# Kernel optimization log

Hardware: AMD Instinct MI355X
Metric: run time of the kernel (lower is better)

## Reference

```python
import jax, jax.numpy as jnp
import numpy as np

N_NODES = 50000
N_EDGES = 1000000
IN_SIZE = 64
OUT_SIZE = 64
EDGE_DIM = 16
BN_EPS = 1e-5
GIN_EPS = 0.0  # GINEConv default eps, train_eps=False


def setup_inputs() -> dict:
    key = jax.random.key(0)
    ks = jax.random.split(key, 10)
    s = 1.0 / np.sqrt(IN_SIZE)
    return {
        "x": jax.random.normal(ks[0], (N_NODES, IN_SIZE), dtype=jnp.float32),
        "edge_index": jax.random.randint(ks[1], (2, N_EDGES), 0, N_NODES, dtype=jnp.int64),
        "edge_attr": jax.random.normal(ks[2], (N_EDGES, EDGE_DIM), dtype=jnp.float32),
        # GINEConv internal edge projection Linear(edge_dim -> in_size)
        "W_edge": jax.random.uniform(ks[3], (IN_SIZE, EDGE_DIM), jnp.float32, -s, s),
        "b_edge": jnp.zeros((IN_SIZE,), jnp.float32),
        # MLP: Linear(in, out) -> BatchNorm1d(out) -> ReLU -> Linear(out, out)
        "W1": jax.random.uniform(ks[4], (OUT_SIZE, IN_SIZE), jnp.float32, -s, s),
        "b1": jnp.zeros((OUT_SIZE,), jnp.float32),
        "gamma": jnp.ones((OUT_SIZE,), jnp.float32),
        "beta": jnp.zeros((OUT_SIZE,), jnp.float32),
        "W2": jax.random.uniform(ks[5], (OUT_SIZE, OUT_SIZE), jnp.float32, -1.0 / np.sqrt(OUT_SIZE), 1.0 / np.sqrt(OUT_SIZE)),
        "b2": jnp.zeros((OUT_SIZE,), jnp.float32),
    }


def reference(x, edge_index, edge_attr, W_edge, b_edge, W1, b1, gamma, beta, W2, b2):
    src = edge_index[0]  # x_j (message source)
    dst = edge_index[1]  # aggregation target
    # project edge attrs to node-feature dim (GINEConv's self.lin)
    ea = edge_attr @ W_edge.T + b_edge                      # [E, d]
    msg = jax.nn.relu(x[src] + ea)                          # [E, d]
    agg = jax.ops.segment_sum(msg, dst, num_segments=x.shape[0])  # [N, d]
    h = (1.0 + GIN_EPS) * x + agg                           # GINE combine
    # MLP with BatchNorm1d (training mode: batch stats, biased var)
    h = h @ W1.T + b1
    mean = jnp.mean(h, axis=0)
    var = jnp.var(h, axis=0)
    h = gamma * (h - mean) * jax.lax.rsqrt(var + BN_EPS) + beta
    h = jax.nn.relu(h)
    return h @ W2.T + b2
```

## Files before the change

### kernel.cpp

```cpp
#include <hip/hip_runtime.h>
#include <hip/hip_fp16.h>

#define NN 50000
#define NE 1000000
#define D  64
#define ED 16
#define CAP 64
#define BN_EPS 1e-5f
#define QSCALE 1048576.0f

#define BSH  8
#define NBKT 196
#define BCAP 6144
#define EPB  4096

struct alignas(16) SE8  { int   v[8];  };
struct alignas(16) F16v { float f[16]; };

__global__ __launch_bounds__(256) void xhalf_kernel(
    const float* __restrict__ x, __half* __restrict__ xh)
{
    const int i = blockIdx.x * 256 + threadIdx.x;
    if (i >= NN * D / 4) return;
    const float4 a = reinterpret_cast<const float4*>(x)[i];
    ushort4 h;
    h.x = __half_as_ushort(__float2half(a.x));
    h.y = __half_as_ushort(__float2half(a.y));
    h.z = __half_as_ushort(__float2half(a.z));
    h.w = __half_as_ushort(__float2half(a.w));
    reinterpret_cast<ushort4*>(xh)[i] = h;
}

__global__ __launch_bounds__(256) void partA_kernel(
    const int*  __restrict__ ei32,
    int*        __restrict__ gcur,
    uint2*      __restrict__ bucketed)
{
    __shared__ uint2 s_staged[EPB];
    __shared__ int s_cnt[NBKT], s_pref[NBKT], s_cnt2[NBKT], s_gbase[NBKT];

    const int tid = threadIdx.x;
    const long long base = (long long)blockIdx.x * EPB;
    const int nedge = (int)((NE - base < EPB) ? (NE - base) : EPB);

    const int hi = ei32[2 * (tid & 63) + 1];
    const bool is64 = !__any(hi != 0);

    for (int i = tid; i < NBKT; i += 256) { s_cnt[i] = 0; s_cnt2[i] = 0; }
    __syncthreads();

    int srcv[16], dstv[16];
    #pragma unroll
    for (int i = 0; i < 16; ++i) {
        const int k = i * 256 + tid;
        int s = 0, d = 0;
        if (k < nedge) {
            const long long e = base + k;
            s = is64 ? ei32[2 * e]        : ei32[e];
            d = is64 ? ei32[2 * (NE + e)] : ei32[NE + e];
            atomicAdd(&s_cnt[d >> BSH], 1);
        }
        srcv[i] = s; dstv[i] = d;
    }
    __syncthreads();

    if (tid < NBKT) s_pref[tid] = s_cnt[tid];
    __syncthreads();
    for (int off = 1; off < NBKT; off <<= 1) {
        int v = 0;
        if (tid < NBKT && tid >= off) v = s_pref[tid - off];
        __syncthreads();
        if (tid < NBKT) s_pref[tid] += v;
        __syncthreads();
    }
    if (tid < NBKT) s_gbase[tid] = atomicAdd(&gcur[tid], s_cnt[tid]);
    __syncthreads();

    #pragma unroll
    for (int i = 0; i < 16; ++i) {
        const int k = i * 256 + tid;
        if (k < nedge) {
            const int d = dstv[i], b = d >> BSH;
            const int r = atomicAdd(&s_cnt2[b], 1);
            const int p = (s_pref[b] - s_cnt[b]) + r;
            s_staged[p] = make_uint2((unsigned)srcv[i] | ((unsigned)d << 16),
                                     (unsigned)(base + k));
        }
    }
    __syncthreads();

    for (int p = tid; p < nedge; p += 256) {
        const uint2 rec = s_staged[p];
        const int d = (int)(rec.x >> 16), b = d >> BSH;
        const int local = p - (s_pref[b] - s_cnt[b]);
        const int gpos = s_gbase[b] + local;
        if (gpos < BCAP)
            bucketed[(size_t)b * BCAP + gpos] = rec;
    }
}

__global__ __launch_bounds__(512) void partB_kernel(
    const uint2* __restrict__ bucketed,
    const int*   __restrict__ gcur,
    int*         __restrict__ cursor,
    int2*        __restrict__ padded)
{
    __shared__ int s_deg[1 << BSH];
    const int tid = threadIdx.x;
    const int b = blockIdx.x;

    for (int i = tid; i < (1 << BSH); i += 512) s_deg[i] = 0;
    __syncthreads();

    const int cnt = min(gcur[b], BCAP);
    const uint2* reg = bucketed + (size_t)b * BCAP;
    for (int k = tid; k < cnt; k += 512) {
        const uint2 rec = reg[k];
        const int src = (int)(rec.x & 0xffffu);
        const int dst = (int)(rec.x >> 16);
        const int slot = atomicAdd(&s_deg[dst & ((1 << BSH) - 1)], 1);
        if (slot < CAP)
            padded[(size_t)dst * CAP + slot] = make_int2(src, (int)rec.y);
    }
    __syncthreads();
    for (int i = tid; i < (1 << BSH); i += 512) {
        const int n = (b << BSH) + i;
        if (n < NN) cursor[n] = s_deg[i];
    }
}

__global__ __launch_bounds__(256) void scatter_kernel(
    const int* __restrict__ ei32,
    int*       __restrict__ cursor,
    int2*      __restrict__ padded)
{
    const int e = blockIdx.x * 256 + threadIdx.x;
    const int hi = ei32[2 * (threadIdx.x & 63) + 1];
    const bool is64 = !__any(hi != 0);
    if (e >= NE) return;
    const int src = is64 ? ei32[2 * e]        : ei32[e];
    const int dst = is64 ? ei32[2 * (NE + e)] : ei32[NE + e];
    const int slot = atomicAdd(&cursor[dst], 1);
    if (slot < CAP) padded[(size_t)dst * CAP + slot] = make_int2(src, e);
}

template<bool XH>
__global__ __launch_bounds__(256) void gather_kernel(
    const int2*  __restrict__ padded,
    const int*   __restrict__ cursor,
    const float* __restrict__ x,
    const __half* __restrict__ xh,
    const float* __restrict__ ea,
    const float* __restrict__ W_edge,
    const float* __restrict__ b_edge,
    float*       __restrict__ agg,
    int n0, int n1)
{
    const int tid  = threadIdx.x;
    const int lane = tid & 63;
    const int n = __builtin_amdgcn_readfirstlane(n0 + blockIdx.x * 4 + (tid >> 6));
    if (n >= n1) return;

    float wv[ED];
    #pragma unroll
    for (int i = 0; i < ED / 4; ++i) {
        float4 t = reinterpret_cast<const float4*>(W_edge)[lane * (ED / 4) + i];
        wv[4*i+0] = t.x; wv[4*i+1] = t.y; wv[4*i+2] = t.z; wv[4*i+3] = t.w;
    }
    const float bo = b_edge[lane];

    const int deg = __builtin_amdgcn_readfirstlane(min(cursor[n], CAP));
    const int2* row = padded + (size_t)n * CAP;

    int iacc = 0;
    for (int e0 = 0; e0 < deg; e0 += 4) {
        const SE8 g = *reinterpret_cast<const SE8*>(row + e0);

        const bool l1 = (e0 + 1 < deg), l2 = (e0 + 2 < deg), l3 = (e0 + 3 < deg);
        const int src0 = __builtin_amdgcn_readfirstlane(g.v[0]);
        const int eid0 = __builtin_amdgcn_readfirstlane(g.v[1]);
        const int src1 = __builtin_amdgcn_readfirstlane(l1 ? g.v[2] : g.v[0]);
        const int eid1 = __builtin_amdgcn_readfirstlane(l1 ? g.v[3] : g.v[1]);
        const int src2 = __builtin_amdgcn_readfirstlane(l2 ? g.v[4] : g.v[0]);
        const int eid2 = __builtin_amdgcn_readfirstlane(l2 ? g.v[5] : g.v[1]);
        const int src3 = __builtin_amdgcn_readfirstlane(l3 ? g.v[6] : g.v[0]);
        const int eid3 = __builtin_amdgcn_readfirstlane(l3 ? g.v[7] : g.v[1]);

        const F16v a0 = *reinterpret_cast<const F16v*>(ea + (size_t)eid0 * ED);
        const F16v a1 = *reinterpret_cast<const F16v*>(ea + (size_t)eid1 * ED);
        const F16v a2 = *reinterpret_cast<const F16v*>(ea + (size_t)eid2 * ED);
        const F16v a3 = *reinterpret_cast<const F16v*>(ea + (size_t)eid3 * ED);

        float xv0, xv1, xv2, xv3;
        if (XH) {
            xv0 = __half2float(xh[(size_t)src0 * D + lane]);
            xv1 = __half2float(xh[(size_t)src1 * D + lane]);
            xv2 = __half2float(xh[(size_t)src2 * D + lane]);
            xv3 = __half2float(xh[(size_t)src3 * D + lane]);
        } else {
            xv0 = x[(size_t)src0 * D + lane];
            xv1 = x[(size_t)src1 * D + lane];
            xv2 = x[(size_t)src2 * D + lane];
            xv3 = x[(size_t)src3 * D + lane];
        }

        float d0 = bo, d1 = bo, d2 = bo, d3 = bo;
        #pragma unroll
        for (int k = 0; k < ED; ++k) {
            d0 += a0.f[k] * wv[k];
            d1 += a1.f[k] * wv[k];
            d2 += a2.f[k] * wv[k];
            d3 += a3.f[k] * wv[k];
        }
        iacc += __float2int_rn(fmaxf(d0 + xv0, 0.f) * QSCALE);
        iacc += l1 ? __float2int_rn(fmaxf(d1 + xv1, 0.f) * QSCALE) : 0;
        iacc += l2 ? __float2int_rn(fmaxf(d2 + xv2, 0.f) * QSCALE) : 0;
        iacc += l3 ? __float2int_rn(fmaxf(d3 + xv3, 0.f) * QSCALE) : 0;
    }
    agg[(size_t)n * D + lane] = (float)iacc * (1.0f / QSCALE);
}

__global__ __launch_bounds__(256) void edge_kernel(
    const float* __restrict__ x,
    const int*   __restrict__ ei32,
    const float* __restrict__ ea,
    const float* __restrict__ W_edge,
    const float* __restrict__ b_edge,
    float*       __restrict__ agg)
{
    __shared__ float s_ea[64 * ED];
    __shared__ int   s_src[64];
    __shared__ int   s_dst[64];

    const int tid  = threadIdx.x;
    const int lane = tid & 63;
    const int wave = tid >> 6;
    const long long ebase = (long long)blockIdx.x * 64;

    const int hi = ei32[2 * lane + 1];
    const bool is64 = !__any(hi != 0);

    float w[ED];
    #pragma unroll
    for (int i = 0; i < ED / 4; ++i) {
        float4 t = reinterpret_cast<const float4*>(W_edge)[lane * (ED / 4) + i];
        w[4*i+0] = t.x; w[4*i+1] = t.y; w[4*i+2] = t.z; w[4*i+3] = t.w;
    }
    const float bo = b_edge[lane];

    reinterpret_cast<float4*>(s_ea)[tid] =
        reinterpret_cast<const float4*>(ea + ebase * ED)[tid];

    if (tid < 64) {
        long long e = ebase + tid;
        s_src[tid] = is64 ? ei32[2 * e] : ei32[e];
    } else if (tid < 128) {
        long long e = ebase + (tid - 64);
        s_dst[tid - 64] = is64 ? ei32[2 * (NE + e)] : ei32[NE + e];
    }
    __syncthreads();

    #pragma unroll 4
    for (int i = 0; i < 16; ++i) {
        const int el = wave * 16 + i;
        float acc = bo;
        const float* er = s_ea + el * ED;
        #pragma unroll
        for (int k = 0; k < ED; ++k) acc += er[k] * w[k];
        const long long s = s_src[el];
        const long long d = s_dst[el];
        float m = fmaxf(acc + x[s * D + lane], 0.f);
        atomicAdd(&agg[d * D + lane], m);
    }
}


__global__ __launch_bounds__(256) void node1_kernel(
    const float* __restrict__ x,
    const float* __restrict__ agg,
    const float* __restrict__ W1,
    const float* __restrict__ b1,
    float*       __restrict__ h1,
    float*       __restrict__ colsum,
    float*       __restrict__ colsumsq)
{
    __shared__ float s_h[64 * D];
    const int tid  = threadIdx.x;
    const int o    = tid & 63;
    const int wave = tid >> 6;
    const long long rbase = (long long)blockIdx.x * 64;

    float w[D];
    #pragma unroll
    for (int i = 0; i < D / 4; ++i) {
        float4 t = reinterpret_cast<const float4*>(W1)[o * (D / 4) + i];
        w[4*i+0] = t.x; w[4*i+1] = t.y; w[4*i+2] = t.z; w[4*i+3] = t.w;
    }

    #pragma unroll
    for (int i = 0; i < 4; ++i) {
        const int f4 = tid + 256 * i;
        const long long row = rbase + (f4 >> 4);
        float4 t = make_float4(0.f, 0.f, 0.f, 0.f);
        if (row < NN) {
            float4 a = reinterpret_cast<const float4*>(x)  [row * (D/4) + (f4 & 15)];
            float4 g = reinterpret_cast<const float4*>(agg)[row * (D/4) + (f4 & 15)];
            t.x = a.x + g.x; t.y = a.y + g.y; t.z = a.z + g.z; t.w = a.w + g.w;
        }
        reinterpret_cast<float4*>(s_h)[f4] = t;
    }
    __syncthreads();

    const float bb = b1[o];
    float psum = 0.f, psq = 0.f;
    for (int i = 0; i < 16; ++i) {
        const int r = wave + 4 * i;
        const long long row = rbase + r;
        float acc = bb;
        const float4* sr = reinterpret_cast<const float4*>(s_h + r * D);
        #pragma unroll
        for (int k = 0; k < D / 4; ++k) {
            float4 v = sr[k];
            acc += v.x * w[4*k+0] + v.y * w[4*k+1] + v.z * w[4*k+2] + v.w * w[4*k+3];
        }
        if (row < NN) {
            h1[row * D + o] = acc;
            psum += acc;
            psq  += acc * acc;
        }
    }
    __syncthreads();
    s_h[wave * 64 + o]       = psum;
    s_h[256 + wave * 64 + o] = psq;
    __syncthreads();
    if (tid < 64) {
        float s0 = s_h[tid] + s_h[64 + tid] + s_h[128 + tid] + s_h[192 + tid];
        float q0 = s_h[256 + tid] + s_h[320 + tid] + s_h[384 + tid] + s_h[448 + tid];
        atomicAdd(&colsum[tid], s0);
        atomicAdd(&colsumsq[tid], q0);
    }
}

__global__ void bnstats_kernel(
    const float* __restrict__ colsum,
    const float* __restrict__ colsumsq,
    const float* __restrict__ gamma,
    const float* __restrict__ beta,
    float*       __restrict__ scale,
    float*       __restrict__ shift)
{
    const int o = threadIdx.x;
    const float inv_n = 1.f / (float)NN;
    const float mean = colsum[o] * inv_n;
    const float var  = colsumsq[o] * inv_n - mean * mean;
    const float sc   = gamma[o] * rsqrtf(var + BN_EPS);
    scale[o] = sc;
    shift[o] = beta[o] - mean * sc;
}

__global__ __launch_bounds__(256) void node2_kernel(
    const float* __restrict__ h1,
    const float* __restrict__ scale,
    const float* __restrict__ shift,
    const float* __restrict__ W2,
    const float* __restrict__ b2,
    float*       __restrict__ out)
{
    __shared__ float s_a[64 * D];
    __shared__ float s_sc[D];
    __shared__ float s_sh[D];
    const int tid  = threadIdx.x;
    const int o    = tid & 63;
    const int wave = tid >> 6;
    const long long rbase = (long long)blockIdx.x * 64;

    if (tid < D) { s_sc[tid] = scale[tid]; s_sh[tid] = shift[tid]; }

    float w[D];
    #pragma unroll
    for (int i = 0; i < D / 4; ++i) {
        float4 t = reinterpret_cast<const float4*>(W2)[o * (D / 4) + i];
        w[4*i+0] = t.x; w[4*i+1] = t.y; w[4*i+2] = t.z; w[4*i+3] = t.w;
    }
    __syncthreads();

    #pragma unroll
    for (int i = 0; i < 4; ++i) {
        const int f4 = tid + 256 * i;
        const long long row = rbase + (f4 >> 4);
        float4 t = make_float4(0.f, 0.f, 0.f, 0.f);
        if (row < NN) {
            float4 v = reinterpret_cast<const float4*>(h1)[row * (D/4) + (f4 & 15)];
            const int c = (f4 & 15) * 4;
            t.x = fmaxf(v.x * s_sc[c+0] + s_sh[c+0], 0.f);
            t.y = fmaxf(v.y * s_sc[c+1] + s_sh[c+1], 0.f);
            t.z = fmaxf(v.z * s_sc[c+2] + s_sh[c+2], 0.f);
            t.w = fmaxf(v.w * s_sc[c+3] + s_sh[c+3], 0.f);
        }
        reinterpret_cast<float4*>(s_a)[f4] = t;
    }
    __syncthreads();

    const float bb = b2[o];
    for (int i = 0; i < 16; ++i) {
        const int r = wave + 4 * i;
        const long long row = rbase + r;
        float acc = bb;
        const float4* sr = reinterpret_cast<const float4*>(s_a + r * D);
        #pragma unroll
        for (int k = 0; k < D / 4; ++k) {
            float4 v = sr[k];
            acc += v.x * w[4*k+0] + v.y * w[4*k+1] + v.z * w[4*k+2] + v.w * w[4*k+3];
        }
        if (row < NN) out[row * D + o] = acc;
    }
}


extern "C" void kernel_launch(void* const* d_in, const int* in_sizes, int n_in,
                              void* d_out, int out_size, void* d_ws, size_t ws_size,
                              hipStream_t stream)
{
    const float* x      = (const float*)d_in[0];
    const int*   ei32   = (const int*)  d_in[1];
    const float* ea     = (const float*)d_in[2];
    const float* W_edge = (const float*)d_in[3];
    const float* b_edge = (const float*)d_in[4];
    const float* W1     = (const float*)d_in[5];
    const float* b1     = (const float*)d_in[6];
    const float* gamma  = (const float*)d_in[7];
    const float* beta   = (const float*)d_in[8];
    const float* W2     = (const float*)d_in[9];
    const float* b2     = (const float*)d_in[10];
    float* out = (float*)d_out;

    float*  agg      = (float*)d_ws;
    float*  h1       = agg + (size_t)NN * D;
    int*    cursor   = (int*)(h1 + (size_t)NN * D);
    float*  colsum   = (float*)(cursor + NN);
    float*  colsumsq = colsum + 64;
    float*  scale    = colsumsq + 64;
    float*  shift    = scale + 64;
    int2*   padded   = (int2*)(shift + 64);
    __half* xh       = (__half*)(padded + (size_t)NN * CAP);
    int*    gcur     = (int*)(xh + (size_t)NN * D);
    uint2*  bucketed = (uint2*)h1;

    const size_t need_base = (size_t)(2 * NN * D + NN + 256) * 4 + (size_t)NN * CAP * 8;
    const size_t need_xh   = need_base + (size_t)NN * D * 2;
    const size_t need_rx   = need_xh + (size_t)NBKT * 4;

    if (ws_size >= need_rx) {
        hipMemsetAsync(gcur, 0, (size_t)NBKT * 4, stream);
        hipMemsetAsync(colsum, 0, 256 * 4, stream);
        xhalf_kernel<<<(NN * D / 4 + 255) / 256, 256, 0, stream>>>(x, xh);
        partA_kernel<<<(NE + EPB - 1) / EPB, 256, 0, stream>>>(ei32, gcur, bucketed);
        partB_kernel<<<NBKT, 512, 0, stream>>>(bucketed, gcur, cursor, padded);
        gather_kernel<true><<<NN / 8, 256, 0, stream>>>(padded, cursor, x, xh, ea, W_edge, b_edge, agg, 0, NN / 2);
        gather_kernel<true><<<NN / 8, 256, 0, stream>>>(padded, cursor, x, xh, ea, W_edge, b_edge, agg, NN / 2, NN);
    } else if (ws_size >= need_base) {
        hipMemsetAsync(cursor, 0, (size_t)(NN + 256) * 4, stream);
        scatter_kernel<<<(NE + 255) / 256, 256, 0, stream>>>(ei32, cursor, padded);
        gather_kernel<false><<<NN / 8, 256, 0, stream>>>(padded, cursor, x, xh, ea, W_edge, b_edge, agg, 0, NN / 2);
        gather_kernel<false><<<NN / 8, 256, 0, stream>>>(padded, cursor, x, xh, ea, W_edge, b_edge, agg, NN / 2, NN);
    } else {
        hipMemsetAsync(agg, 0, (size_t)NN * D * 4, stream);
        hipMemsetAsync(cursor, 0, (size_t)(NN + 256) * 4, stream);
        edge_kernel<<<NE / 64, 256, 0, stream>>>(x, ei32, ea, W_edge, b_edge, agg);
    }
    node1_kernel<<<(NN + 63) / 64, 256, 0, stream>>>(x, agg, W1, b1, h1, colsum, colsumsq);
    bnstats_kernel<<<1, 64, 0, stream>>>(colsum, colsumsq, gamma, beta, scale, shift);
    node2_kernel<<<(NN + 63) / 64, 256, 0, stream>>>(h1, scale, shift, W2, b2, out);
}
```

Measured before the change: 172.3 us.

## Pack edge attrs to fp16, use fdot2 gather with software pipelining, finer buckets

Adds a pack kernel that converts both x and edge_attr to fp16 in one pass. A new gather kernel reads the fp16 edge attributes and computes the edge projection with packed fp16 dot products, double-buffering the loads of the next edge group. It also halves the bucket width and edges-per-block in the radix partition, launches partA with 512 threads, and merges the two half-range gather launches into one. The intent is to cut the gather's memory traffic and instruction count, at the cost of an extra full pass over edge_attr, more workspace, and reduced precision in the edge projection.

```diff
diff --git a/kernel.cpp b/kernel.cpp
--- a/kernel.cpp
+++ b/kernel.cpp
@@ -9,13 +9,44 @@
 #define BN_EPS 1e-5f
 #define QSCALE 1048576.0f
 
-#define BSH  8
-#define NBKT 196
-#define BCAP 6144
-#define EPB  4096
-
-struct alignas(16) SE8  { int   v[8];  };
+#define BSH  7
+#define NBKT 391
+#define BCAP 3072
+#define EPB  2048
+
+typedef _Float16 f16;
+typedef _Float16 f16x2 __attribute__((ext_vector_type(2)));
+
+struct alignas(16) SE8  { int v[8]; };
+struct alignas(16) H16  { unsigned u[8]; };
 struct alignas(16) F16v { float f[16]; };
+
+__global__ __launch_bounds__(256) void pack_kernel(
+    const float* __restrict__ x, const float* __restrict__ ea,
+    __half* __restrict__ xh, __half* __restrict__ eah)
+{
+    const long long NX  = (long long)NN * D / 4;
+    const long long NEA = (long long)NE * ED / 4;
+    const long long i = (long long)blockIdx.x * 256 + threadIdx.x;
+    if (i < NX) {
+        const float4 a = reinterpret_cast<const float4*>(x)[i];
+        ushort4 h;
+        h.x = __half_as_ushort(__float2half(a.x));
+        h.y = __half_as_ushort(__float2half(a.y));
+        h.z = __half_as_ushort(__float2half(a.z));
+        h.w = __half_as_ushort(__float2half(a.w));
+        reinterpret_cast<ushort4*>(xh)[i] = h;
+    } else if (i < NX + NEA) {
+        const long long j = i - NX;
+        const float4 a = reinterpret_cast<const float4*>(ea)[j];
+        ushort4 h;
+        h.x = __half_as_ushort(__float2half(a.x));
+        h.y = __half_as_ushort(__float2half(a.y));
+        h.z = __half_as_ushort(__float2half(a.z));
+        h.w = __half_as_ushort(__float2half(a.w));
+        reinterpret_cast<ushort4*>(eah)[j] = h;
+    }
+}
 
 __global__ __launch_bounds__(256) void xhalf_kernel(
     const float* __restrict__ x, __half* __restrict__ xh)
@@ -31,7 +62,7 @@
     reinterpret_cast<ushort4*>(xh)[i] = h;
 }
 
-__global__ __launch_bounds__(256) void partA_kernel(
+__global__ __launch_bounds__(512) void partA_kernel(
     const int*  __restrict__ ei32,
     int*        __restrict__ gcur,
     uint2*      __restrict__ bucketed)
@@ -41,18 +72,18 @@
 
     const int tid = threadIdx.x;
     const long long base = (long long)blockIdx.x * EPB;
-    const int nedge = (int)((NE - base < EPB) ? (NE - base) : EPB);
+    const int nedge = (int)(((long long)NE - base < EPB) ? (NE - base) : EPB);
 
     const int hi = ei32[2 * (tid & 63) + 1];
     const bool is64 = !__any(hi != 0);
 
-    for (int i = tid; i < NBKT; i += 256) { s_cnt[i] = 0; s_cnt2[i] = 0; }
-    __syncthreads();
-
-    int srcv[16], dstv[16];
-    #pragma unroll
-    for (int i = 0; i < 16; ++i) {
-        const int k = i * 256 + tid;
+    for (int i = tid; i < NBKT; i += 512) { s_cnt[i] = 0; s_cnt2[i] = 0; }
+    __syncthreads();
+
+    int srcv[4], dstv[4];
+    #pragma unroll
+    for (int i = 0; i < 4; ++i) {
+        const int k = i * 512 + tid;
         int s = 0, d = 0;
         if (k < nedge) {
             const long long e = base + k;
@@ -77,8 +108,8 @@
     __syncthreads();
 
     #pragma unroll
-    for (int i = 0; i < 16; ++i) {
-        const int k = i * 256 + tid;
+    for (int i = 0; i < 4; ++i) {
+        const int k = i * 512 + tid;
         if (k < nedge) {
             const int d = dstv[i], b = d >> BSH;
             const int r = atomicAdd(&s_cnt2[b], 1);
@@ -89,7 +120,7 @@
     }
     __syncthreads();
 
-    for (int p = tid; p < nedge; p += 256) {
+    for (int p = tid; p < nedge; p += 512) {
         const uint2 rec = s_staged[p];
         const int d = (int)(rec.x >> 16), b = d >> BSH;
         const int local = p - (s_pref[b] - s_cnt[b]);
@@ -144,6 +175,79 @@
     if (slot < CAP) padded[(size_t)dst * CAP + slot] = make_int2(src, e);
 }
 
+__global__ __launch_bounds__(256) void gather2_kernel(
+    const int2*   __restrict__ padded,
+    const int*    __restrict__ cursor,
+    const __half* __restrict__ xh,
+    const __half* __restrict__ eah,
+    const float*  __restrict__ W_edge,
+    const float*  __restrict__ b_edge,
+    float*        __restrict__ agg)
+{
+    const int tid  = threadIdx.x;
+    const int lane = tid & 63;
+    const int n = __builtin_amdgcn_readfirstlane(blockIdx.x * 4 + (tid >> 6));
+    if (n >= NN) return;
+
+    f16x2 wp[8];
+    #pragma unroll
+    for (int i = 0; i < 8; ++i) {
+        const float2 t = reinterpret_cast<const float2*>(W_edge)[lane * 8 + i];
+        f16x2 p; p.x = (f16)t.x; p.y = (f16)t.y;
+        wp[i] = p;
+    }
+    const float bo = b_edge[lane];
+
+    const int deg = __builtin_amdgcn_readfirstlane(min(cursor[n], CAP));
+    const int2* row = padded + (size_t)n * CAP;
+    if (deg <= 0) { agg[(size_t)n * D + lane] = 0.f; return; }
+    const int G = (deg + 3) >> 2;
+
+    auto LD_SE = [&](int g) -> SE8 {
+        return *reinterpret_cast<const SE8*>(row + g * 4);
+    };
+    auto LD_GRP = [&](const SE8& s, int g, H16 at[4], float xv[4]) {
+        #pragma unroll
+        for (int j = 0; j < 4; ++j) {
+            const bool lj = (g * 4 + j) < deg;
+            const int sj = __builtin_amdgcn_readfirstlane(lj ? s.v[2*j]   : s.v[0]);
+            const int ej = __builtin_amdgcn_readfirstlane(lj ? s.v[2*j+1] : s.v[1]);
+            at[j] = *reinterpret_cast<const H16*>(eah + (size_t)ej * ED);
+            xv[j] = __half2float(xh[(size_t)sj * D + lane]);
+        }
+    };
+    auto COMP = [&](const H16 at[4], const float xv[4], int g, int& iacc) {
+        #pragma unroll
+        for (int j = 0; j < 4; ++j) {
+            const bool lj = (g * 4 + j) < deg;
+            float d = bo;
+            #pragma unroll
+            for (int k = 0; k < 8; ++k)
+                d = __builtin_amdgcn_fdot2(__builtin_bit_cast(f16x2, at[j].u[k]),
+                                           wp[k], d, false);
+            const float m = fmaxf(d + xv[j], 0.f);
+            iacc += lj ? __float2int_rn(m * QSCALE) : 0;
+        }
+    };
+
+    int iacc = 0;
+    H16 atA[4], atB[4];
+    float xvA[4], xvB[4];
+    SE8 sB = LD_SE(0);
+    LD_GRP(sB, 0, atA, xvA);
+    if (G > 1) sB = LD_SE(1);
+
+    for (int g = 0; g < G; g += 2) {
+        if (g + 1 < G) LD_GRP(sB, g + 1, atB, xvB);
+        if (g + 2 < G) sB = LD_SE(g + 2);
+        COMP(atA, xvA, g, iacc);
+        if (g + 2 < G) LD_GRP(sB, g + 2, atA, xvA);
+        if (g + 3 < G) sB = LD_SE(g + 3);
+        if (g + 1 < G) COMP(atB, xvB, g + 1, iacc);
+    }
+    agg[(size_t)n * D + lane] = (float)iacc * (1.0f / QSCALE);
+}
+
 template<bool XH>
 __global__ __launch_bounds__(256) void gather_kernel(
     const int2*  __restrict__ padded,
@@ -153,13 +257,12 @@
     const float* __restrict__ ea,
     const float* __restrict__ W_edge,
     const float* __restrict__ b_edge,
-    float*       __restrict__ agg,
-    int n0, int n1)
+    float*       __restrict__ agg)
 {
     const int tid  = threadIdx.x;
     const int lane = tid & 63;
-    const int n = __builtin_amdgcn_readfirstlane(n0 + blockIdx.x * 4 + (tid >> 6));
-    if (n >= n1) return;
+    const int n = __builtin_amdgcn_readfirstlane(blockIdx.x * 4 + (tid >> 6));
+    if (n >= NN) return;
 
     float wv[ED];
     #pragma unroll
@@ -175,7 +278,6 @@
     int iacc = 0;
     for (int e0 = 0; e0 < deg; e0 += 4) {
         const SE8 g = *reinterpret_cast<const SE8*>(row + e0);
-
         const bool l1 = (e0 + 1 < deg), l2 = (e0 + 2 < deg), l3 = (e0 + 3 < deg);
         const int src0 = __builtin_amdgcn_readfirstlane(g.v[0]);
         const int eid0 = __builtin_amdgcn_readfirstlane(g.v[1]);
@@ -442,27 +544,37 @@
     float*  scale    = colsumsq + 64;
     float*  shift    = scale + 64;
     int2*   padded   = (int2*)(shift + 64);
-    __half* xh       = (__half*)(padded + (size_t)NN * CAP);
-    int*    gcur     = (int*)(xh + (size_t)NN * D);
+    __half* eah      = (__half*)(padded + (size_t)NN * CAP);
+    __half* xh_full  = (__half*)(eah + (size_t)NE * ED);
+    __half* xh_small = (__half*)eah;
     uint2*  bucketed = (uint2*)h1;
 
     const size_t need_base = (size_t)(2 * NN * D + NN + 256) * 4 + (size_t)NN * CAP * 8;
-    const size_t need_xh   = need_base + (size_t)NN * D * 2;
-    const size_t need_rx   = need_xh + (size_t)NBKT * 4;
-
-    if (ws_size >= need_rx) {
+    const size_t need_t2   = need_base + (size_t)NN * D * 2 + (size_t)NBKT * 4;
+    const size_t need_t1   = need_base + (size_t)NE * ED * 2 + (size_t)NN * D * 2 + (size_t)NBKT * 4;
+
+    if (ws_size >= need_t1) {
+        __half* xh   = xh_full;
+        int*    gcur = (int*)(xh + (size_t)NN * D);
+        hipMemsetAsync(gcur, 0, (size_t)NBKT * 4, stream);
+        hipMemsetAsync(colsum, 0, 256 * 4, stream);
+        pack_kernel<<<(NN * D / 4 + NE * ED / 4 + 255) / 256, 256, 0, stream>>>(x, ea, xh, eah);
+        partA_kernel<<<(NE + EPB - 1) / EPB, 512, 0, stream>>>(ei32, gcur, bucketed);
+        partB_kernel<<<NBKT, 512, 0, stream>>>(bucketed, gcur, cursor, padded);
+        gather2_kernel<<<(NN + 3) / 4, 256, 0, stream>>>(padded, cursor, xh, eah, W_edge, b_edge, agg);
+    } else if (ws_size >= need_t2) {
+        __half* xh   = xh_small;
+        int*    gcur = (int*)(xh + (size_t)NN * D);
         hipMemsetAsync(gcur, 0, (size_t)NBKT * 4, stream);
         hipMemsetAsync(colsum, 0, 256 * 4, stream);
         xhalf_kernel<<<(NN * D / 4 + 255) / 256, 256, 0, stream>>>(x, xh);
-        partA_kernel<<<(NE + EPB - 1) / EPB, 256, 0, stream>>>(ei32, gcur, bucketed);
+        partA_kernel<<<(NE + EPB - 1) / EPB, 512, 0, stream>>>(ei32, gcur, bucketed);
         partB_kernel<<<NBKT, 512, 0, stream>>>(bucketed, gcur, cursor, padded);
-        gather_kernel<true><<<NN / 8, 256, 0, stream>>>(padded, cursor, x, xh, ea, W_edge, b_edge, agg, 0, NN / 2);
-        gather_kernel<true><<<NN / 8, 256, 0, stream>>>(padded, cursor, x, xh, ea, W_edge, b_edge, agg, NN / 2, NN);
+        gather_kernel<true><<<(NN + 3) / 4, 256, 0, stream>>>(padded, cursor, x, xh, ea, W_edge, b_edge, agg);
     } else if (ws_size >= need_base) {
         hipMemsetAsync(cursor, 0, (size_t)(NN + 256) * 4, stream);
         scatter_kernel<<<(NE + 255) / 256, 256, 0, stream>>>(ei32, cursor, padded);
-        gather_kernel<false><<<NN / 8, 256, 0, stream>>>(padded, cursor, x, xh, ea, W_edge, b_edge, agg, 0, NN / 2);
-        gather_kernel<false><<<NN / 8, 256, 0, stream>>>(padded, cursor, x, xh, ea, W_edge, b_edge, agg, NN / 2, NN);
+        gather_kernel<false><<<(NN + 3) / 4, 256, 0, stream>>>(padded, cursor, x, (const __half*)eah, ea, W_edge, b_edge, agg);
     } else {
         hipMemsetAsync(agg, 0, (size_t)NN * D * 4, stream);
         hipMemsetAsync(cursor, 0, (size_t)(NN + 256) * 4, stream);
```

New measurement: 198.5 us. 1.15x slower.

## Replace two-pass padded CSR build with bucketed fp16 edge attrs and shared-memory aggregation

Applied to the files above, without the earlier changes.

The partition kernel now packs each edge's attributes into fp16 in bucket order alongside the src/dst word. This removes the second pass that built the padded per-node adjacency list. A new gather kernel processes one 128-node bucket per block, streams the bucketed edges contiguously, computes the edge projection with fp16 dot2 instructions, and accumulates into shared memory with fixed-point integer atomics. This cuts random reads of edge_attr and the padded-list writes, at the cost of fp16 precision on edge attributes and weights, heavy LDS atomic contention, and silently dropping edges if a bucket exceeds its capacity.

```diff
diff --git a/kernel.cpp b/kernel.cpp
--- a/kernel.cpp
+++ b/kernel.cpp
@@ -9,12 +9,16 @@
 #define BN_EPS 1e-5f
 #define QSCALE 1048576.0f
 
-#define BSH  8
-#define NBKT 196
-#define BCAP 6144
-#define EPB  4096
-
-struct alignas(16) SE8  { int   v[8];  };
+#define BSH  7
+#define NBKT 391
+#define BCAP 3072
+#define EPB2 4096
+
+typedef _Float16 f16;
+typedef _Float16 f16x2 __attribute__((ext_vector_type(2)));
+
+struct alignas(16) SE8  { int v[8]; };
+struct alignas(16) H16  { unsigned u[8]; };
 struct alignas(16) F16v { float f[16]; };
 
 __global__ __launch_bounds__(256) void xhalf_kernel(
@@ -31,28 +35,31 @@
     reinterpret_cast<ushort4*>(xh)[i] = h;
 }
 
-__global__ __launch_bounds__(256) void partA_kernel(
-    const int*  __restrict__ ei32,
-    int*        __restrict__ gcur,
-    uint2*      __restrict__ bucketed)
-{
-    __shared__ uint2 s_staged[EPB];
+__global__ __launch_bounds__(512) void partA2_kernel(
+    const int*   __restrict__ ei32,
+    const float* __restrict__ ea,
+    int*         __restrict__ gcur,
+    unsigned*    __restrict__ bse,
+    __half*      __restrict__ battr)
+{
+    __shared__ unsigned       s_se[EPB2];
+    __shared__ unsigned short s_k[EPB2];
     __shared__ int s_cnt[NBKT], s_pref[NBKT], s_cnt2[NBKT], s_gbase[NBKT];
 
     const int tid = threadIdx.x;
-    const long long base = (long long)blockIdx.x * EPB;
-    const int nedge = (int)((NE - base < EPB) ? (NE - base) : EPB);
+    const long long base = (long long)blockIdx.x * EPB2;
+    const int nedge = (int)(((long long)NE - base < EPB2) ? (NE - base) : EPB2);
 
     const int hi = ei32[2 * (tid & 63) + 1];
     const bool is64 = !__any(hi != 0);
 
-    for (int i = tid; i < NBKT; i += 256) { s_cnt[i] = 0; s_cnt2[i] = 0; }
-    __syncthreads();
-
-    int srcv[16], dstv[16];
-    #pragma unroll
-    for (int i = 0; i < 16; ++i) {
-        const int k = i * 256 + tid;
+    for (int i = tid; i < NBKT; i += 512) { s_cnt[i] = 0; s_cnt2[i] = 0; }
+    __syncthreads();
+
+    int srcv[8], dstv[8];
+    #pragma unroll
+    for (int i = 0; i < 8; ++i) {
+        const int k = i * 512 + tid;
         int s = 0, d = 0;
         if (k < nedge) {
             const long long e = base + k;
@@ -77,55 +84,142 @@
     __syncthreads();
 
     #pragma unroll
-    for (int i = 0; i < 16; ++i) {
-        const int k = i * 256 + tid;
+    for (int i = 0; i < 8; ++i) {
+        const int k = i * 512 + tid;
         if (k < nedge) {
             const int d = dstv[i], b = d >> BSH;
             const int r = atomicAdd(&s_cnt2[b], 1);
             const int p = (s_pref[b] - s_cnt[b]) + r;
-            s_staged[p] = make_uint2((unsigned)srcv[i] | ((unsigned)d << 16),
-                                     (unsigned)(base + k));
-        }
-    }
-    __syncthreads();
-
-    for (int p = tid; p < nedge; p += 256) {
-        const uint2 rec = s_staged[p];
-        const int d = (int)(rec.x >> 16), b = d >> BSH;
-        const int local = p - (s_pref[b] - s_cnt[b]);
-        const int gpos = s_gbase[b] + local;
-        if (gpos < BCAP)
-            bucketed[(size_t)b * BCAP + gpos] = rec;
-    }
-}
-
-__global__ __launch_bounds__(512) void partB_kernel(
-    const uint2* __restrict__ bucketed,
-    const int*   __restrict__ gcur,
-    int*         __restrict__ cursor,
-    int2*        __restrict__ padded)
-{
-    __shared__ int s_deg[1 << BSH];
-    const int tid = threadIdx.x;
-    const int b = blockIdx.x;
-
-    for (int i = tid; i < (1 << BSH); i += 512) s_deg[i] = 0;
-    __syncthreads();
-
-    const int cnt = min(gcur[b], BCAP);
-    const uint2* reg = bucketed + (size_t)b * BCAP;
-    for (int k = tid; k < cnt; k += 512) {
-        const uint2 rec = reg[k];
-        const int src = (int)(rec.x & 0xffffu);
-        const int dst = (int)(rec.x >> 16);
-        const int slot = atomicAdd(&s_deg[dst & ((1 << BSH) - 1)], 1);
-        if (slot < CAP)
-            padded[(size_t)dst * CAP + slot] = make_int2(src, (int)rec.y);
-    }
-    __syncthreads();
-    for (int i = tid; i < (1 << BSH); i += 512) {
-        const int n = (b << BSH) + i;
-        if (n < NN) cursor[n] = s_deg[i];
+            s_se[p] = (unsigned)srcv[i] | ((unsigned)d << 16);
+            s_k[p]  = (unsigned short)k;
+        }
+    }
+    __syncthreads();
+
+    for (int p = tid; p < nedge; p += 512) {
+        const unsigned se = s_se[p];
+        const int k = s_k[p];
+        const int d = (int)(se >> 16), b = d >> BSH;
+        const int gpos = s_gbase[b] + (p - (s_pref[b] - s_cnt[b]));
+        if (gpos < BCAP) {
+            bse[(size_t)b * BCAP + gpos] = se;
+            const float4* er = reinterpret_cast<const float4*>(ea + (base + k) * ED);
+            float f[16];
+            *reinterpret_cast<float4*>(f + 0)  = er[0];
+            *reinterpret_cast<float4*>(f + 4)  = er[1];
+            *reinterpret_cast<float4*>(f + 8)  = er[2];
+            *reinterpret_cast<float4*>(f + 12) = er[3];
+            unsigned u[8];
+            #pragma unroll
+            for (int q = 0; q < 8; ++q) {
+                const unsigned lo = __half_as_ushort(__float2half(f[2*q]));
+                const unsigned hh = __half_as_ushort(__float2half(f[2*q+1]));
+                u[q] = lo | (hh << 16);
+            }
+            uint4* dst = reinterpret_cast<uint4*>(battr + ((size_t)b * BCAP + gpos) * ED);
+            dst[0] = make_uint4(u[0], u[1], u[2], u[3]);
+            dst[1] = make_uint4(u[4], u[5], u[6], u[7]);
+        }
+    }
+}
+
+__global__ __launch_bounds__(256) void gather3_kernel(
+    const unsigned* __restrict__ bse,
+    const __half*   __restrict__ battr,
+    const int*      __restrict__ gcur,
+    const __half*   __restrict__ xh,
+    const float*    __restrict__ W_edge,
+    const float*    __restrict__ b_edge,
+    float*          __restrict__ agg)
+{
+    __shared__ int s_acc[128 * 64];
+    const int tid  = threadIdx.x;
+    const int lane = tid & 63;
+    const int w    = tid >> 6;
+    const int b    = blockIdx.x;
+
+    for (int i = tid; i < 128 * 64; i += 256) s_acc[i] = 0;
+
+    f16x2 wp[8];
+    #pragma unroll
+    for (int i = 0; i < 8; ++i) {
+        const float2 t = reinterpret_cast<const float2*>(W_edge)[lane * 8 + i];
+        f16x2 p; p.x = (f16)t.x; p.y = (f16)t.y;
+        wp[i] = p;
+    }
+    const float bo = b_edge[lane];
+    __syncthreads();
+
+    const int cnt = __builtin_amdgcn_readfirstlane(min(gcur[b], BCAP));
+    const int chunk4 = ((cnt + 15) >> 4) << 2;
+    const int wstart = w * chunk4;
+    const int wend   = min(wstart + chunk4, cnt);
+
+    const unsigned* rowse = bse   + (size_t)b * BCAP;
+    const __half*   rowat = battr + (size_t)b * BCAP * ED;
+
+    if (wend > wstart) {
+        const int G = (wend - wstart + 3) >> 2;
+
+        auto LD_SE = [&](int g) -> uint4 {
+            return *reinterpret_cast<const uint4*>(rowse + wstart + g * 4);
+        };
+        auto LD_GRP = [&](const uint4& s4, int g, H16 at[4], float xv[4],
+                          int dl[4], bool lv[4]) {
+            #pragma unroll
+            for (int j = 0; j < 4; ++j) {
+                const int idx = wstart + g * 4 + j;
+                const bool lj = idx < wend;
+                const unsigned sj = (j == 0) ? s4.x : (j == 1) ? s4.y
+                                 : (j == 2) ? s4.z : s4.w;
+                const unsigned se = lj ? sj : s4.x;
+                const int src = __builtin_amdgcn_readfirstlane((int)(se & 0xffffu));
+                dl[j] = __builtin_amdgcn_readfirstlane((int)((se >> 16) & 127u));
+                const int ii = lj ? idx : (wstart + g * 4);
+                at[j] = *reinterpret_cast<const H16*>(rowat + (size_t)ii * ED);
+                xv[j] = __half2float(xh[(size_t)src * D + lane]);
+                lv[j] = lj;
+            }
+        };
+        auto COMP = [&](const H16 at[4], const float xv[4],
+                        const int dl[4], const bool lv[4]) {
+            #pragma unroll
+            for (int j = 0; j < 4; ++j) {
+                if (lv[j]) {
+                    float d = bo;
+                    #pragma unroll
+                    for (int k = 0; k < 8; ++k)
+                        d = __builtin_amdgcn_fdot2(
+                                __builtin_bit_cast(f16x2, at[j].u[k]), wp[k], d, false);
+                    const float m = fmaxf(d + xv[j], 0.f);
+                    atomicAdd(&s_acc[dl[j] * 64 + lane], __float2int_rn(m * QSCALE));
+                }
+            }
+        };
+
+        H16 atA[4], atB[4];
+        float xvA[4], xvB[4];
+        int dlA[4], dlB[4];
+        bool lvA[4], lvB[4];
+        uint4 sB = LD_SE(0);
+        LD_GRP(sB, 0, atA, xvA, dlA, lvA);
+        if (G > 1) sB = LD_SE(1);
+
+        for (int g = 0; g < G; g += 2) {
+            if (g + 1 < G) LD_GRP(sB, g + 1, atB, xvB, dlB, lvB);
+            if (g + 2 < G) sB = LD_SE(g + 2);
+            COMP(atA, xvA, dlA, lvA);
+            if (g + 2 < G) LD_GRP(sB, g + 2, atA, xvA, dlA, lvA);
+            if (g + 3 < G) sB = LD_SE(g + 3);
+            if (g + 1 < G) COMP(atB, xvB, dlB, lvB);
+        }
+    }
+    __syncthreads();
+
+    const float inv = 1.0f / QSCALE;
+    for (int r = w; r < 128; r += 4) {
+        const int n = (b << BSH) + r;
+        if (n < NN) agg[(size_t)n * D + lane] = (float)s_acc[r * 64 + lane] * inv;
     }
 }
 
@@ -153,13 +247,12 @@
     const float* __restrict__ ea,
     const float* __restrict__ W_edge,
     const float* __restrict__ b_edge,
-    float*       __restrict__ agg,
-    int n0, int n1)
+    float*       __restrict__ agg)
 {
     const int tid  = threadIdx.x;
     const int lane = tid & 63;
-    const int n = __builtin_amdgcn_readfirstlane(n0 + blockIdx.x * 4 + (tid >> 6));
-    if (n >= n1) return;
+    const int n = __builtin_amdgcn_readfirstlane(blockIdx.x * 4 + (tid >> 6));
+    if (n >= NN) return;
 
     float wv[ED];
     #pragma unroll
@@ -175,7 +268,6 @@
     int iacc = 0;
     for (int e0 = 0; e0 < deg; e0 += 4) {
         const SE8 g = *reinterpret_cast<const SE8*>(row + e0);
-
         const bool l1 = (e0 + 1 < deg), l2 = (e0 + 2 < deg), l3 = (e0 + 3 < deg);
         const int src0 = __builtin_amdgcn_readfirstlane(g.v[0]);
         const int eid0 = __builtin_amdgcn_readfirstlane(g.v[1]);
@@ -434,41 +526,56 @@
     const float* b2     = (const float*)d_in[10];
     float* out = (float*)d_out;
 
-    float*  agg      = (float*)d_ws;
-    float*  h1       = agg + (size_t)NN * D;
-    int*    cursor   = (int*)(h1 + (size_t)NN * D);
-    float*  colsum   = (float*)(cursor + NN);
-    float*  colsumsq = colsum + 64;
-    float*  scale    = colsumsq + 64;
-    float*  shift    = scale + 64;
-    int2*   padded   = (int2*)(shift + 64);
-    __half* xh       = (__half*)(padded + (size_t)NN * CAP);
-    int*    gcur     = (int*)(xh + (size_t)NN * D);
-    uint2*  bucketed = (uint2*)h1;
-
+    float*    agg      = (float*)d_ws;
+    float*    h1       = agg + (size_t)NN * D;
+    float*    colsum   = h1 + (size_t)NN * D;
+    float*    colsumsq = colsum + 64;
+    float*    scale    = colsumsq + 64;
+    float*    shift    = scale + 64;
+    unsigned* bse      = (unsigned*)(shift + 64);
+    __half*   battr    = (__half*)(bse + (size_t)NBKT * BCAP);
+    __half*   xh       = battr + (size_t)NBKT * BCAP * ED;
+    int*      gcur     = (int*)(xh + (size_t)NN * D);
+
+    const size_t need_t1 = (size_t)(2 * NN * D + 256) * 4
+                         + (size_t)NBKT * BCAP * 4
+                         + (size_t)NBKT * BCAP * ED * 2
+                         + (size_t)NN * D * 2 + (size_t)NBKT * 4;
+
+    int*    f_cursor = (int*)(h1 + (size_t)NN * D);
+    float*  f_colsum = (float*)(f_cursor + NN);
+    int2*   f_padded = (int2*)(f_colsum + 256);
+    __half* f_xh     = (__half*)(f_padded + (size_t)NN * CAP);
     const size_t need_base = (size_t)(2 * NN * D + NN + 256) * 4 + (size_t)NN * CAP * 8;
-    const size_t need_xh   = need_base + (size_t)NN * D * 2;
-    const size_t need_rx   = need_xh + (size_t)NBKT * 4;
-
-    if (ws_size >= need_rx) {
+    const size_t need_t2   = need_base + (size_t)NN * D * 2;
+
+    if (ws_size >= need_t1) {
         hipMemsetAsync(gcur, 0, (size_t)NBKT * 4, stream);
         hipMemsetAsync(colsum, 0, 256 * 4, stream);
         xhalf_kernel<<<(NN * D / 4 + 255) / 256, 256, 0, stream>>>(x, xh);
-        partA_kernel<<<(NE + EPB - 1) / EPB, 256, 0, stream>>>(ei32, gcur, bucketed);
-        partB_kernel<<<NBKT, 512, 0, stream>>>(bucketed, gcur, cursor, padded);
-        gather_kernel<true><<<NN / 8, 256, 0, stream>>>(padded, cursor, x, xh, ea, W_edge, b_edge, agg, 0, NN / 2);
-        gather_kernel<true><<<NN / 8, 256, 0, stream>>>(padded, cursor, x, xh, ea, W_edge, b_edge, agg, NN / 2, NN);
+        partA2_kernel<<<(NE + EPB2 - 1) / EPB2, 512, 0, stream>>>(ei32, ea, gcur, bse, battr);
+        gather3_kernel<<<NBKT, 256, 0, stream>>>(bse, battr, gcur, xh, W_edge, b_edge, agg);
+        node1_kernel<<<(NN + 63) / 64, 256, 0, stream>>>(x, agg, W1, b1, h1, colsum, colsumsq);
+        bnstats_kernel<<<1, 64, 0, stream>>>(colsum, colsumsq, gamma, beta, scale, shift);
+        node2_kernel<<<(NN + 63) / 64, 256, 0, stream>>>(h1, scale, shift, W2, b2, out);
+        return;
+    }
+
+    if (ws_size >= need_t2) {
+        hipMemsetAsync(f_cursor, 0, (size_t)(NN + 256) * 4, stream);
+        xhalf_kernel<<<(NN * D / 4 + 255) / 256, 256, 0, stream>>>(x, f_xh);
+        scatter_kernel<<<(NE + 255) / 256, 256, 0, stream>>>(ei32, f_cursor, f_padded);
+        gather_kernel<true><<<(NN + 3) / 4, 256, 0, stream>>>(f_padded, f_cursor, x, f_xh, ea, W_edge, b_edge, agg);
     } else if (ws_size >= need_base) {
-        hipMemsetAsync(cursor, 0, (size_t)(NN + 256) * 4, stream);
-        scatter_kernel<<<(NE + 255) / 256, 256, 0, stream>>>(ei32, cursor, padded);
-        gather_kernel<false><<<NN / 8, 256, 0, stream>>>(padded, cursor, x, xh, ea, W_edge, b_edge, agg, 0, NN / 2);
-        gather_kernel<false><<<NN / 8, 256, 0, stream>>>(padded, cursor, x, xh, ea, W_edge, b_edge, agg, NN / 2, NN);
+        hipMemsetAsync(f_cursor, 0, (size_t)(NN + 256) * 4, stream);
+        scatter_kernel<<<(NE + 255) / 256, 256, 0, stream>>>(ei32, f_cursor, f_padded);
+        gather_kernel<false><<<(NN + 3) / 4, 256, 0, stream>>>(f_padded, f_cursor, x, f_xh, ea, W_edge, b_edge, agg);
     } else {
         hipMemsetAsync(agg, 0, (size_t)NN * D * 4, stream);
-        hipMemsetAsync(cursor, 0, (size_t)(NN + 256) * 4, stream);
+        hipMemsetAsync(f_cursor, 0, (size_t)(NN + 256) * 4, stream);
         edge_kernel<<<NE / 64, 256, 0, stream>>>(x, ei32, ea, W_edge, b_edge, agg);
     }
-    node1_kernel<<<(NN + 63) / 64, 256, 0, stream>>>(x, agg, W1, b1, h1, colsum, colsumsq);
-    bnstats_kernel<<<1, 64, 0, stream>>>(colsum, colsumsq, gamma, beta, scale, shift);
-    node2_kernel<<<(NN + 63) / 64, 256, 0, stream>>>(h1, scale, shift, W2, b2, out);
-}
+    node1_kernel<<<(NN + 63) / 64, 256, 0, stream>>>(x, agg, W1, b1, h1, f_colsum, f_colsum + 64);
+    bnstats_kernel<<<1, 64, 0, stream>>>(f_colsum, f_colsum + 64, gamma, beta, f_colsum + 128, f_colsum + 192);
+    node2_kernel<<<(NN + 63) / 64, 256, 0, stream>>>(h1, f_colsum + 128, f_colsum + 192, W2, b2, out);
+}
```

Measured after the change: 269.1 us. 1.56x slower.
